# Kernel optimization log

Measured on AMD Instinct MI355X. Metric: run time of the kernel, lower is better.

The kernel has to match this reference:

```python
import jax, jax.numpy as jnp
import numpy as np

S, N, A = 64, 4096, 32
HID, DM, NH, DK = 256, 128, 4, 32
EPS = 1e-5
SCALE = float(np.sqrt(DK))


def setup_inputs() -> dict:
    key = jax.random.key(0)
    ks = jax.random.split(key, 20)
    w = lambda i, sh: jax.random.normal(ks[i], sh, jnp.float32) * 0.02
    z = lambda n: jnp.zeros((n,), jnp.float32)
    return {
        "agent_states": jax.random.normal(ks[0], (N, S), jnp.float32),
        "sw1": w(1, (N * S, HID)), "sb1": z(HID),
        "sw2": w(2, (HID, HID)), "sb2": z(HID),
        "sow": w(3, (HID, 64)), "sob": z(64),
        "tw": w(4, (S + 64, DM)), "tb": z(DM),
        "wq": w(5, (DM, DM)), "bq": z(DM),
        "wk": w(6, (DM, DM)), "bk": z(DM),
        "wv": w(7, (DM, DM)), "bv": z(DM),
        "wo": w(8, (DM, DM)), "bo": z(DM),
        "ln_g": jnp.ones((DM,), jnp.float32), "ln_b": z(DM),
        "taw1": w(9, (DM, 64)), "tab1": z(64),
        "taw2": w(10, (64, 32)), "tab2": z(32),
        "ow1": w(11, (S + DM + 32, 256)), "ob1": z(256),
        "ow2": w(12, (256, DM)), "ob2": z(DM),
        "aw": w(13, (DM, A)), "ab": z(A),
        "vw": w(14, (DM, 1)), "vb": z(1),
        "cw": w(15, (S, 64)), "cb": z(64),
        "cdw": w(16, (64, 32)), "cdb": z(32),
    }


def reference(agent_states, sw1, sb1, sw2, sb2, sow, sob, tw, tb,
              wq, bq, wk, bk, wv, bv, wo, bo, ln_g, ln_b,
              taw1, tab1, taw2, tab2, ow1, ob1, ow2, ob2,
              aw, ab, vw, vb, cw, cb, cdw, cdb):
    n = agent_states.shape[0]
    # strategic level: flatten all agent states -> global objective [64]
    gs = agent_states.reshape(-1)
    strat = jax.nn.relu(jax.nn.relu(gs @ sw1 + sb1) @ sw2 + sb2)
    gobj = strat @ sow + sob
    # tactical encode (batched over agents instead of Python loop)
    tact_in = jnp.concatenate(
        [agent_states, jnp.broadcast_to(gobj, (n, gobj.shape[0]))], axis=-1)
    tact = jax.nn.relu(tact_in @ tw + tb)[None]  # [1, n, DM]
    # multi-head attention across agents
    q = (tact @ wq + bq).reshape(1, n, NH, DK).transpose(0, 2, 1, 3)
    k = (tact @ wk + bk).reshape(1, n, NH, DK).transpose(0, 2, 1, 3)
    v = (tact @ wv + bv).reshape(1, n, NH, DK).transpose(0, 2, 1, 3)
    scores = jnp.einsum('bhqd,bhkd->bhqk', q, k) / SCALE
    attn = jax.nn.softmax(scores, axis=-1)  # [1, NH, n, n]
    ctx = jnp.einsum('bhqk,bhkd->bhqd', attn, v).transpose(0, 2, 1, 3).reshape(1, n, DM)
    res = ctx @ wo + bo + tact
    mu = res.mean(-1, keepdims=True)
    var = res.var(-1, keepdims=True)  # biased, like torch LayerNorm
    coord = ((res - mu) / jnp.sqrt(var + EPS) * ln_g + ln_b)[0]  # [n, DM]
    # task allocation (softmax over 32 tasks)
    task = jax.nn.softmax(jax.nn.relu(coord @ taw1 + tab1) @ taw2 + tab2, axis=-1)
    # operational level -> actions / values
    op_in = jnp.concatenate([agent_states, coord, task], axis=-1)
    opf = jax.nn.relu(jax.nn.relu(op_in @ ow1 + ob1) @ ow2 + ob2)
    actions = opf @ aw + ab
    values = opf @ vw + vb
    # communication messages (two stacked linears, no activation in source)
    messages = (agent_states @ cw + cb) @ cdw + cdb
    return actions, values, messages, task, attn, gobj
```

## Files before the change

kernel.cpp:

```cpp
#include <hip/hip_runtime.h>

typedef __attribute__((ext_vector_type(8))) short s8v;
typedef __attribute__((ext_vector_type(4))) float f4v;

#define MFMA16(a, b, c) __builtin_amdgcn_mfma_f32_16x16x32_bf16((a), (b), (c), 0, 0, 0)

#define NAG   4096
#define SDIM  64
#define DMOD  128
#define NHD   4
#define DKD   32
#define HIDD  256
static constexpr float INV_SCALE = 0.17677669529663687f;
static constexpr float EPSV = 1e-5f;

#define OFF_ACT   0
#define OFF_VAL   131072
#define OFF_MSG   135168
#define OFF_TASK  266240
#define OFF_ATTN  397312
#define OFF_GOBJ  67506176

static constexpr size_t WS_P1   = 0;
static constexpr size_t WS_P1B  = 524288;
static constexpr size_t WS_P2   = 540672;
static constexpr size_t WS_TACT = 558080;
static constexpr size_t WS_Q    = 2655232;
static constexpr size_t WS_K    = 3703808;
static constexpr size_t WS_VT   = 4752384;
static constexpr size_t WS_CTX  = 5800960;
static constexpr size_t WS_OPIN = 7898112;
static constexpr size_t WS_H    = 9733120;
static constexpr size_t WS_OPF  = 11830272;
static constexpr size_t WS_OW1T = 12878848;
static constexpr size_t WS_OW2T = 12993536;

typedef unsigned short u16;
typedef unsigned int   u32;

static __device__ __forceinline__ u16 f2bf(float f) {
    union { float f; u32 u; } x; x.f = f;
    u32 r = x.u + 0x7FFFu + ((x.u >> 16) & 1u);
    return (u16)(r >> 16);
}
static __device__ __forceinline__ float bf2f(u16 b) {
    union { u32 u; float f; } x; x.u = ((u32)b) << 16;
    return x.f;
}

__global__ void kw_prep(const float* __restrict__ ow1, const float* __restrict__ ow2,
                        u16* __restrict__ w1t, u16* __restrict__ w2t) {
    int tid = threadIdx.x;
    int b = blockIdx.x;
    if (b < 224) {
        w1t[tid * 224 + b] = f2bf(ow1[b * 256 + tid]);
    } else {
        if (tid < 128) {
            int k0 = (b - 224) * 8;
#pragma unroll
            for (int kk = 0; kk < 8; ++kk) {
                int k = k0 + kk;
                w2t[tid * 256 + k] = f2bf(ow2[k * 128 + tid]);
            }
        }
    }
}

__global__ __launch_bounds__(256) void k1_sw1(const float* __restrict__ gs,
                                              const float* __restrict__ sw1,
                                              float* __restrict__ p1) {
    __shared__ float gsl[512];
    __shared__ float red[4][256];
    int tid = threadIdx.x;
    int b = blockIdx.x;
    gsl[tid]       = gs[b * 512 + tid];
    gsl[tid + 256] = gs[b * 512 + 256 + tid];
    __syncthreads();
    int t = tid & 63;
    int rg = tid >> 6;
    const f4v* w4 = (const f4v*)sw1;
    f4v acc = {0.f, 0.f, 0.f, 0.f};
    size_t rb = (size_t)b * 512;
#pragma unroll 4
    for (int r = rg; r < 512; r += 4) {
        float g = gsl[r];
        f4v w = __builtin_nontemporal_load(&w4[(rb + r) * 64 + t]);
        acc[0] += g * w[0]; acc[1] += g * w[1]; acc[2] += g * w[2]; acc[3] += g * w[3];
    }
    red[rg][4 * t + 0] = acc[0]; red[rg][4 * t + 1] = acc[1];
    red[rg][4 * t + 2] = acc[2]; red[rg][4 * t + 3] = acc[3];
    __syncthreads();
    float s = red[0][tid] + red[1][tid] + red[2][tid] + red[3][tid];
    p1[b * 256 + tid] = s;
}

__global__ void k1b_red(const float* __restrict__ p1, float* __restrict__ p1b) {
    int j = threadIdx.x;
    int b0 = blockIdx.x * 32;
    float s = 0.f;
#pragma unroll
    for (int b = 0; b < 32; ++b) s += p1[(b0 + b) * 256 + j];
    p1b[blockIdx.x * 256 + j] = s;
}

__global__ void k2b_strat(const float* __restrict__ p1b, const float* __restrict__ sb1,
                          const float* __restrict__ sw2, float* __restrict__ p2) {
    __shared__ float h1[256];
    int j = threadIdx.x;
    float s = 0.f;
#pragma unroll
    for (int b = 0; b < 16; ++b) s += p1b[b * 256 + j];
    h1[j] = fmaxf(s + sb1[j], 0.f);
    __syncthreads();
    int i0 = blockIdx.x * 16;
    float acc = 0.f;
#pragma unroll
    for (int i = 0; i < 16; ++i) acc += h1[i0 + i] * sw2[(i0 + i) * 256 + j];
    p2[blockIdx.x * 256 + j] = acc;
}

__global__ __launch_bounds__(256) void k3_tact_qkv(
    const float* __restrict__ p2, const float* __restrict__ sb2,
    const float* __restrict__ sow, const float* __restrict__ sob,
    const float* __restrict__ as, const float* __restrict__ tw, const float* __restrict__ tb,
    const float* __restrict__ wq, const float* __restrict__ bq,
    const float* __restrict__ wk, const float* __restrict__ bk,
    const float* __restrict__ wv, const float* __restrict__ bv,
    float* __restrict__ out_gobj, float* __restrict__ tactws,
    u16* __restrict__ qws, u16* __restrict__ kws, u16* __restrict__ vtws) {
    __shared__ float strat[256];
    __shared__ float gobj[64];
    __shared__ float asl[16][64];
    __shared__ float tl[16][128];
    int tid = threadIdx.x;
    int a0 = blockIdx.x * 16;
    {
        float s = 0.f;
#pragma unroll
        for (int b = 0; b < 16; ++b) s += p2[b * 256 + tid];
        strat[tid] = fmaxf(s + sb2[tid], 0.f);
    }
#pragma unroll
    for (int r = 0; r < 4; ++r) {
        int idx = tid + r * 256;
        asl[idx >> 6][idx & 63] = as[a0 * 64 + idx];
    }
    __syncthreads();
    if (tid < 64) {
        float g = sob[tid];
        for (int i = 0; i < 256; ++i) g += strat[i] * sow[i * 64 + tid];
        gobj[tid] = g;
        if (blockIdx.x == 0) out_gobj[tid] = g;
    }
    __syncthreads();
    int ah = tid >> 7, j = tid & 127;
    float gacc = 0.f;
    for (int i = 0; i < 64; ++i) gacc += gobj[i] * tw[(64 + i) * 128 + j];
    float acc[8];
    float base = tb[j] + gacc;
#pragma unroll
    for (int a = 0; a < 8; ++a) acc[a] = base;
    for (int i = 0; i < 64; ++i) {
        float w = tw[i * 128 + j];
#pragma unroll
        for (int a = 0; a < 8; ++a) acc[a] += asl[ah * 8 + a][i] * w;
    }
#pragma unroll
    for (int a = 0; a < 8; ++a) {
        float t = fmaxf(acc[a], 0.f);
        tl[ah * 8 + a][j] = t;
        tactws[(size_t)(a0 + ah * 8 + a) * 128 + j] = t;
    }
    __syncthreads();
    int h = j >> 5, d = j & 31;
#pragma unroll
    for (int a = 0; a < 8; ++a) acc[a] = 0.f;
    for (int i = 0; i < 128; ++i) {
        float w = wq[i * 128 + j];
#pragma unroll
        for (int a = 0; a < 8; ++a) acc[a] += tl[ah * 8 + a][i] * w;
    }
#pragma unroll
    for (int a = 0; a < 8; ++a)
        qws[h * 131072 + (a0 + ah * 8 + a) * 32 + d] = f2bf((acc[a] + bq[j]) * INV_SCALE);
#pragma unroll
    for (int a = 0; a < 8; ++a) acc[a] = 0.f;
    for (int i = 0; i < 128; ++i) {
        float w = wk[i * 128 + j];
#pragma unroll
        for (int a = 0; a < 8; ++a) acc[a] += tl[ah * 8 + a][i] * w;
    }
#pragma unroll
    for (int a = 0; a < 8; ++a)
        kws[h * 131072 + (a0 + ah * 8 + a) * 32 + d] = f2bf(acc[a] + bk[j]);
#pragma unroll
    for (int a = 0; a < 8; ++a) acc[a] = 0.f;
    for (int i = 0; i < 128; ++i) {
        float w = wv[i * 128 + j];
#pragma unroll
        for (int a = 0; a < 8; ++a) acc[a] += tl[ah * 8 + a][i] * w;
    }
    union { u16 u[8]; s8v v; } pk;
#pragma unroll
    for (int a = 0; a < 8; ++a) pk.u[a] = f2bf(acc[a] + bv[j]);
    *(s8v*)(vtws + h * 131072 + d * 4096 + a0 + ah * 8) = pk.v;
}

__global__ __launch_bounds__(256) void k4_attn(
    const u16* __restrict__ qws, const u16* __restrict__ kws, const u16* __restrict__ vtws,
    float* __restrict__ attn, float* __restrict__ ctxws) {
    int tid = threadIdx.x;
    int wid = tid >> 6;
    int l = tid & 63;
    int g = l >> 4;
    int ln = l & 15;
    int h = blockIdx.x >> 8;
    int qt = (blockIdx.x & 255) * 16;
    const u16* qh = qws + h * 131072;
    const u16* kh = kws + h * 131072;
    const u16* vh = vtws + h * 131072;
    int j0 = wid * 1024;

    s8v aq = *(const s8v*)(qh + (qt + ln) * 32 + 8 * g);
    f4v zero = {0.f, 0.f, 0.f, 0.f};

    __shared__ float red[4][16];
    __shared__ __align__(16) u16 ldsPb[4][2][16][40];
    __shared__ float pctx[4][16][32];

    f4v lacc = zero, accA = zero, accB = zero;
    int buf = 0;
    for (int jc = 0; jc < 32; ++jc) {
        int jb = j0 + jc * 32;
        s8v b0 = *(const s8v*)(kh + (jb + ln) * 32 + 8 * g);
        s8v b1 = *(const s8v*)(kh + (jb + 16 + ln) * 32 + 8 * g);
        f4v S0 = MFMA16(aq, b0, zero);
        f4v S1 = MFMA16(aq, b1, zero);
#pragma unroll
        for (int r = 0; r < 4; ++r) {
            float w0 = __expf(S0[r]);
            float w1 = __expf(S1[r]);
            lacc[r] += w0 + w1;
            ldsPb[wid][buf][4 * g + r][ln] = f2bf(w0);
            ldsPb[wid][buf][4 * g + r][16 + ln] = f2bf(w1);
        }
        s8v bp = *(const s8v*)&ldsPb[wid][buf][ln][8 * g];
        s8v va = *(const s8v*)(vh + ln * 4096 + jb + 8 * g);
        s8v vb = *(const s8v*)(vh + (16 + ln) * 4096 + jb + 8 * g);
        accA = MFMA16(va, bp, accA);
        accB = MFMA16(vb, bp, accB);
        buf ^= 1;
    }
#pragma unroll
    for (int m = 1; m <= 8; m <<= 1) {
        lacc[0] += __shfl_xor(lacc[0], m);
        lacc[1] += __shfl_xor(lacc[1], m);
        lacc[2] += __shfl_xor(lacc[2], m);
        lacc[3] += __shfl_xor(lacc[3], m);
    }
    if (ln == 0) {
#pragma unroll
        for (int r = 0; r < 4; ++r) red[wid][4 * g + r] = lacc[r];
    }
    __syncthreads();
    float linvr[4];
#pragma unroll
    for (int r = 0; r < 4; ++r) {
        int q = 4 * g + r;
        linvr[r] = 1.f / (red[0][q] + red[1][q] + red[2][q] + red[3][q]);
    }
    float linvq = 1.f / (red[0][ln] + red[1][ln] + red[2][ln] + red[3][ln]);
#pragma unroll
    for (int r = 0; r < 4; ++r) {
        pctx[wid][ln][4 * g + r] = accA[r] * linvq;
        pctx[wid][ln][16 + 4 * g + r] = accB[r] * linvq;
    }
    __syncthreads();
    {
        int q = tid >> 4;
        int dp = tid & 15;
#pragma unroll
        for (int dd = 0; dd < 2; ++dd) {
            int d = dp * 2 + dd;
            float s = pctx[0][q][d] + pctx[1][q][d] + pctx[2][q][d] + pctx[3][q][d];
            ctxws[(size_t)(qt + q) * 128 + h * 32 + d] = s;
        }
    }

    float* attnh = attn + (size_t)h * 4096 * 4096;
    s8v b0 = *(const s8v*)(kh + (j0 + ln) * 32 + 8 * g);
    s8v b1 = *(const s8v*)(kh + (j0 + 16 + ln) * 32 + 8 * g);
    for (int jc = 0; jc < 32; ++jc) {
        int jb = j0 + jc * 32;
        int jn = j0 + ((jc + 1) & 31) * 32;
        s8v n0 = *(const s8v*)(kh + (jn + ln) * 32 + 8 * g);
        s8v n1 = *(const s8v*)(kh + (jn + 16 + ln) * 32 + 8 * g);
        f4v S0 = MFMA16(aq, b0, zero);
        f4v S1 = MFMA16(aq, b1, zero);
#pragma unroll
        for (int r = 0; r < 4; ++r) {
            float w0 = __expf(S0[r]) * linvr[r];
            float w1 = __expf(S1[r]) * linvr[r];
            size_t rowo = ((size_t)(qt + 4 * g + r)) * 4096 + jb;
            attnh[rowo + ln] = w0;
            attnh[rowo + 16 + ln] = w1;
        }
        b0 = n0; b1 = n1;
    }
}

__global__ __launch_bounds__(512) void k5_post(
    const float* __restrict__ ctxws, const float* __restrict__ tactws,
    const float* __restrict__ wo, const float* __restrict__ bo,
    const float* __restrict__ lng, const float* __restrict__ lnb,
    const float* __restrict__ taw1, const float* __restrict__ tab1,
    const float* __restrict__ taw2, const float* __restrict__ tab2,
    const float* __restrict__ as, float* __restrict__ dout, u16* __restrict__ opin) {
    __shared__ float wos[128 * 128];
    __shared__ float tw1s[128 * 64];
    __shared__ float tw2s[64 * 32];
    __shared__ float cx[8][128];
    __shared__ float coords[8][128];
    __shared__ float t1v[8][64];
    int tid = threadIdx.x;
    for (int i = tid; i < 128 * 128; i += 512) wos[i] = wo[i];
    for (int i = tid; i < 128 * 64; i += 512) tw1s[i] = taw1[i];
    for (int i = tid; i < 64 * 32; i += 512) tw2s[i] = taw2[i];
    __syncthreads();
    int w = tid >> 6, l = tid & 63;
    for (int it = 0; it < 2; ++it) {
        int n = blockIdx.x * 16 + w * 2 + it;
        float c0 = ctxws[(size_t)n * 128 + l], c1 = ctxws[(size_t)n * 128 + 64 + l];
        float t0 = tactws[(size_t)n * 128 + l], t1 = tactws[(size_t)n * 128 + 64 + l];
        float av = as[n * 64 + l];
        cx[w][l] = c0; cx[w][64 + l] = c1;
        __syncthreads();
        float r0 = bo[l] + t0, r1 = bo[64 + l] + t1;
        for (int k = 0; k < 128; ++k) {
            float cv = cx[w][k];
            r0 += cv * wos[k * 128 + l];
            r1 += cv * wos[k * 128 + 64 + l];
        }
        float s = r0 + r1;
#pragma unroll
        for (int m = 1; m <= 32; m <<= 1) s += __shfl_xor(s, m);
        float mu = s * (1.f / 128.f);
        float d0 = r0 - mu, d1 = r1 - mu;
        float vs = d0 * d0 + d1 * d1;
#pragma unroll
        for (int m = 1; m <= 32; m <<= 1) vs += __shfl_xor(vs, m);
        float rstd = 1.f / sqrtf(vs * (1.f / 128.f) + EPSV);
        float co0 = d0 * rstd * lng[l] + lnb[l];
        float co1 = d1 * rstd * lng[64 + l] + lnb[64 + l];
        coords[w][l] = co0; coords[w][64 + l] = co1;
        opin[(size_t)n * 224 + l] = f2bf(av);
        opin[(size_t)n * 224 + 64 + l] = f2bf(co0);
        opin[(size_t)n * 224 + 128 + l] = f2bf(co1);
        __syncthreads();
        float a1 = tab1[l];
        for (int i = 0; i < 128; ++i) a1 += coords[w][i] * tw1s[i * 64 + l];
        t1v[w][l] = fmaxf(a1, 0.f);
        __syncthreads();
        if (l < 32) {
            float a2 = tab2[l];
            for (int i = 0; i < 64; ++i) a2 += t1v[w][i] * tw2s[i * 32 + l];
            float mx = a2;
#pragma unroll
            for (int m = 1; m <= 16; m <<= 1) mx = fmaxf(mx, __shfl_xor(mx, m));
            float e = __expf(a2 - mx);
            float se = e;
#pragma unroll
            for (int m = 1; m <= 16; m <<= 1) se += __shfl_xor(se, m);
            float tk = e / se;
            dout[OFF_TASK + n * 32 + l] = tk;
            opin[(size_t)n * 224 + 192 + l] = f2bf(tk);
        }
        __syncthreads();
    }
}

__global__ __launch_bounds__(256) void k6a(const u16* __restrict__ opin, const u16* __restrict__ w1t,
                                           const float* __restrict__ ob1, u16* __restrict__ Hws) {
    int tid = threadIdx.x;
    int w = tid >> 6, l = tid & 63, g = l >> 4, ln = l & 15;
    int bm = blockIdx.x & 63, bn = blockIdx.x >> 6;
    int m0 = bm * 64 + w * 16, n0 = bn * 64;
    f4v acc[4];
    f4v zero = {0.f, 0.f, 0.f, 0.f};
#pragma unroll
    for (int nt = 0; nt < 4; ++nt) acc[nt] = zero;
    for (int kt = 0; kt < 7; ++kt) {
        s8v A = *(const s8v*)(opin + (size_t)(m0 + ln) * 224 + kt * 32 + 8 * g);
#pragma unroll
        for (int nt = 0; nt < 4; ++nt) {
            s8v B = *(const s8v*)(w1t + (size_t)(n0 + nt * 16 + ln) * 224 + kt * 32 + 8 * g);
            acc[nt] = MFMA16(A, B, acc[nt]);
        }
    }
#pragma unroll
    for (int nt = 0; nt < 4; ++nt) {
        int col = n0 + nt * 16 + ln;
        float bias = ob1[col];
#pragma unroll
        for (int r = 0; r < 4; ++r) {
            int row = m0 + 4 * g + r;
            Hws[(size_t)row * 256 + col] = f2bf(fmaxf(acc[nt][r] + bias, 0.f));
        }
    }
}

__global__ __launch_bounds__(256) void k6b(const u16* __restrict__ Hws, const u16* __restrict__ w2t,
                                           const float* __restrict__ ob2, u16* __restrict__ opfws) {
    int tid = threadIdx.x;
    int w = tid >> 6, l = tid & 63, g = l >> 4, ln = l & 15;
    int bm = blockIdx.x & 63, bn = blockIdx.x >> 6;
    int m0 = bm * 64 + w * 16, n0 = bn * 64;
    f4v acc[4];
    f4v zero = {0.f, 0.f, 0.f, 0.f};
#pragma unroll
    for (int nt = 0; nt < 4; ++nt) acc[nt] = zero;
    for (int kt = 0; kt < 8; ++kt) {
        s8v A = *(const s8v*)(Hws + (size_t)(m0 + ln) * 256 + kt * 32 + 8 * g);
#pragma unroll
        for (int nt = 0; nt < 4; ++nt) {
            s8v B = *(const s8v*)(w2t + (size_t)(n0 + nt * 16 + ln) * 256 + kt * 32 + 8 * g);
            acc[nt] = MFMA16(A, B, acc[nt]);
        }
    }
#pragma unroll
    for (int nt = 0; nt < 4; ++nt) {
        int col = n0 + nt * 16 + ln;
        float bias = ob2[col];
#pragma unroll
        for (int r = 0; r < 4; ++r) {
            int row = m0 + 4 * g + r;
            opfws[(size_t)row * 128 + col] = f2bf(fmaxf(acc[nt][r] + bias, 0.f));
        }
    }
}

__global__ __launch_bounds__(256) void k6c(const u16* __restrict__ opf, const float* __restrict__ as,
                                           const float* __restrict__ aw, const float* __restrict__ ab,
                                           const float* __restrict__ vw, const float* __restrict__ vb,
                                           const float* __restrict__ cw, const float* __restrict__ cb,
                                           const float* __restrict__ cdw, const float* __restrict__ cdb,
                                           float* __restrict__ dout) {
    __shared__ float opfs[4][128];
    __shared__ float asl[4][64];
    __shared__ float m1s[4][64];
    int tid = threadIdx.x;
    int w = tid >> 6, l = tid & 63;
    int n = blockIdx.x * 4 + w;
    {
        u32 u = *(const u32*)(opf + (size_t)n * 128 + 2 * l);
        opfs[w][2 * l] = bf2f((u16)(u & 0xffff));
        opfs[w][2 * l + 1] = bf2f((u16)(u >> 16));
        asl[w][l] = as[n * 64 + l];
    }
    __syncthreads();
    if (l < 32) {
        float a = ab[l];
        for (int k = 0; k < 128; ++k) a += opfs[w][k] * aw[k * 32 + l];
        dout[OFF_ACT + n * 32 + l] = a;
    }
    {
        float p = opfs[w][l] * vw[l] + opfs[w][64 + l] * vw[64 + l];
#pragma unroll
        for (int m = 1; m <= 32; m <<= 1) p += __shfl_xor(p, m);
        if (l == 0) dout[OFF_VAL + n] = p + vb[0];
    }
    {
        float a = cb[l];
        for (int k = 0; k < 64; ++k) a += asl[w][k] * cw[k * 64 + l];
        m1s[w][l] = a;
    }
    __syncthreads();
    if (l < 32) {
        float a = cdb[l];
        for (int k = 0; k < 64; ++k) a += m1s[w][k] * cdw[k * 32 + l];
        dout[OFF_MSG + n * 32 + l] = a;
    }
}

extern "C" void kernel_launch(void* const* d_in, const int* in_sizes, int n_in,
                              void* d_out, int out_size, void* d_ws, size_t ws_size,
                              hipStream_t stream) {
    const float* as  = (const float*)d_in[0];
    const float* sw1 = (const float*)d_in[1];
    const float* sb1 = (const float*)d_in[2];
    const float* sw2 = (const float*)d_in[3];
    const float* sb2 = (const float*)d_in[4];
    const float* sow = (const float*)d_in[5];
    const float* sob = (const float*)d_in[6];
    const float* tw  = (const float*)d_in[7];
    const float* tb  = (const float*)d_in[8];
    const float* wq  = (const float*)d_in[9];
    const float* bq  = (const float*)d_in[10];
    const float* wk  = (const float*)d_in[11];
    const float* bk  = (const float*)d_in[12];
    const float* wv  = (const float*)d_in[13];
    const float* bv  = (const float*)d_in[14];
    const float* wo  = (const float*)d_in[15];
    const float* bo  = (const float*)d_in[16];
    const float* lng = (const float*)d_in[17];
    const float* lnb = (const float*)d_in[18];
    const float* taw1 = (const float*)d_in[19];
    const float* tab1 = (const float*)d_in[20];
    const float* taw2 = (const float*)d_in[21];
    const float* tab2 = (const float*)d_in[22];
    const float* ow1 = (const float*)d_in[23];
    const float* ob1 = (const float*)d_in[24];
    const float* ow2 = (const float*)d_in[25];
    const float* ob2 = (const float*)d_in[26];
    const float* aw  = (const float*)d_in[27];
    const float* ab  = (const float*)d_in[28];
    const float* vw  = (const float*)d_in[29];
    const float* vb  = (const float*)d_in[30];
    const float* cw  = (const float*)d_in[31];
    const float* cb  = (const float*)d_in[32];
    const float* cdw = (const float*)d_in[33];
    const float* cdb = (const float*)d_in[34];

    float* dout = (float*)d_out;
    char* ws = (char*)d_ws;
    float* p1    = (float*)(ws + WS_P1);
    float* p1b   = (float*)(ws + WS_P1B);
    float* p2    = (float*)(ws + WS_P2);
    float* tactw = (float*)(ws + WS_TACT);
    u16*   qws   = (u16*)(ws + WS_Q);
    u16*   kws   = (u16*)(ws + WS_K);
    u16*   vtws  = (u16*)(ws + WS_VT);
    float* ctxws = (float*)(ws + WS_CTX);
    u16*   opin  = (u16*)(ws + WS_OPIN);
    u16*   Hws   = (u16*)(ws + WS_H);
    u16*   opfws = (u16*)(ws + WS_OPF);
    u16*   w1t   = (u16*)(ws + WS_OW1T);
    u16*   w2t   = (u16*)(ws + WS_OW2T);

    hipLaunchKernelGGL(kw_prep, dim3(256), dim3(256), 0, stream, ow1, ow2, w1t, w2t);
    hipLaunchKernelGGL(k1_sw1, dim3(512), dim3(256), 0, stream, as, sw1, p1);
    hipLaunchKernelGGL(k1b_red, dim3(16), dim3(256), 0, stream, p1, p1b);
    hipLaunchKernelGGL(k2b_strat, dim3(16), dim3(256), 0, stream, p1b, sb1, sw2, p2);
    hipLaunchKernelGGL(k3_tact_qkv, dim3(256), dim3(256), 0, stream,
                       p2, sb2, sow, sob, as, tw, tb, wq, bq, wk, bk, wv, bv,
                       dout + OFF_GOBJ, tactw, qws, kws, vtws);
    hipLaunchKernelGGL(k4_attn, dim3(1024), dim3(256), 0, stream,
                       qws, kws, vtws, dout + OFF_ATTN, ctxws);
    hipLaunchKernelGGL(k5_post, dim3(256), dim3(512), 0, stream,
                       ctxws, tactw, wo, bo, lng, lnb, taw1, tab1, taw2, tab2, as, dout, opin);
    hipLaunchKernelGGL(k6a, dim3(256), dim3(256), 0, stream, opin, w1t, ob1, Hws);
    hipLaunchKernelGGL(k6b, dim3(128), dim3(256), 0, stream, Hws, w2t, ob2, opfws);
    hipLaunchKernelGGL(k6c, dim3(1024), dim3(256), 0, stream,
                       opfws, as, aw, ab, vw, vb, cw, cb, cdw, cdb, dout);
}
```

Measured before the change: 214.8 us.

## Fuse weight prep into sw1 kernel, drop reduce kernel, vectorize attn stores

Folds the ow1/ow2 bf16 transpose prep into extra blocks of the sw1 GEMV kernel. It removes the intermediate partial-sum reduction kernel, so k2b_strat now sums all 512 partials directly. In the attention-probability write loop, the MFMA operand order is swapped so each lane holds four consecutive key columns of one query row, which allows 16-byte vector stores instead of scattered scalar stores. This cuts two launches and should improve store coalescing on the large attn output. The cost is that each of the 16 k2b blocks redundantly reads 512x256 partials.

```diff
diff --git a/kernel.cpp b/kernel.cpp
--- a/kernel.cpp
+++ b/kernel.cpp
@@ -48,31 +48,31 @@
     return x.f;
 }
 
-__global__ void kw_prep(const float* __restrict__ ow1, const float* __restrict__ ow2,
-                        u16* __restrict__ w1t, u16* __restrict__ w2t) {
+__global__ __launch_bounds__(256) void k1_sw1(const float* __restrict__ gs,
+                                              const float* __restrict__ sw1,
+                                              float* __restrict__ p1,
+                                              const float* __restrict__ ow1,
+                                              const float* __restrict__ ow2,
+                                              u16* __restrict__ w1t,
+                                              u16* __restrict__ w2t) {
     int tid = threadIdx.x;
     int b = blockIdx.x;
-    if (b < 224) {
-        w1t[tid * 224 + b] = f2bf(ow1[b * 256 + tid]);
-    } else {
-        if (tid < 128) {
-            int k0 = (b - 224) * 8;
+    if (b >= 512) {
+        int bb = b - 512;
+        if (bb < 224) {
+            w1t[tid * 224 + bb] = f2bf(ow1[bb * 256 + tid]);
+        } else if (tid < 128) {
+            int k0 = (bb - 224) * 8;
 #pragma unroll
             for (int kk = 0; kk < 8; ++kk) {
                 int k = k0 + kk;
                 w2t[tid * 256 + k] = f2bf(ow2[k * 128 + tid]);
             }
         }
-    }
-}
-
-__global__ __launch_bounds__(256) void k1_sw1(const float* __restrict__ gs,
-                                              const float* __restrict__ sw1,
-                                              float* __restrict__ p1) {
+        return;
+    }
     __shared__ float gsl[512];
     __shared__ float red[4][256];
-    int tid = threadIdx.x;
-    int b = blockIdx.x;
     gsl[tid]       = gs[b * 512 + tid];
     gsl[tid + 256] = gs[b * 512 + 256 + tid];
     __syncthreads();
@@ -94,22 +94,13 @@
     p1[b * 256 + tid] = s;
 }
 
-__global__ void k1b_red(const float* __restrict__ p1, float* __restrict__ p1b) {
-    int j = threadIdx.x;
-    int b0 = blockIdx.x * 32;
-    float s = 0.f;
-#pragma unroll
-    for (int b = 0; b < 32; ++b) s += p1[(b0 + b) * 256 + j];
-    p1b[blockIdx.x * 256 + j] = s;
-}
-
-__global__ void k2b_strat(const float* __restrict__ p1b, const float* __restrict__ sb1,
+__global__ void k2b_strat(const float* __restrict__ p1, const float* __restrict__ sb1,
                           const float* __restrict__ sw2, float* __restrict__ p2) {
     __shared__ float h1[256];
     int j = threadIdx.x;
     float s = 0.f;
-#pragma unroll
-    for (int b = 0; b < 16; ++b) s += p1b[b * 256 + j];
+#pragma unroll 8
+    for (int b = 0; b < 512; ++b) s += p1[b * 256 + j];
     h1[j] = fmaxf(s + sb1[j], 0.f);
     __syncthreads();
     int i0 = blockIdx.x * 16;
@@ -263,12 +254,6 @@
         for (int r = 0; r < 4; ++r) red[wid][4 * g + r] = lacc[r];
     }
     __syncthreads();
-    float linvr[4];
-#pragma unroll
-    for (int r = 0; r < 4; ++r) {
-        int q = 4 * g + r;
-        linvr[r] = 1.f / (red[0][q] + red[1][q] + red[2][q] + red[3][q]);
-    }
     float linvq = 1.f / (red[0][ln] + red[1][ln] + red[2][ln] + red[3][ln]);
 #pragma unroll
     for (int r = 0; r < 4; ++r) {
@@ -287,7 +272,7 @@
         }
     }
 
-    float* attnh = attn + (size_t)h * 4096 * 4096;
+    float* rowp = attn + (size_t)h * 4096 * 4096 + (size_t)(qt + ln) * 4096;
     s8v b0 = *(const s8v*)(kh + (j0 + ln) * 32 + 8 * g);
     s8v b1 = *(const s8v*)(kh + (j0 + 16 + ln) * 32 + 8 * g);
     for (int jc = 0; jc < 32; ++jc) {
@@ -295,16 +280,16 @@
         int jn = j0 + ((jc + 1) & 31) * 32;
         s8v n0 = *(const s8v*)(kh + (jn + ln) * 32 + 8 * g);
         s8v n1 = *(const s8v*)(kh + (jn + 16 + ln) * 32 + 8 * g);
-        f4v S0 = MFMA16(aq, b0, zero);
-        f4v S1 = MFMA16(aq, b1, zero);
+        f4v S0 = MFMA16(b0, aq, zero);
+        f4v S1 = MFMA16(b1, aq, zero);
+        f4v o0, o1;
 #pragma unroll
         for (int r = 0; r < 4; ++r) {
-            float w0 = __expf(S0[r]) * linvr[r];
-            float w1 = __expf(S1[r]) * linvr[r];
-            size_t rowo = ((size_t)(qt + 4 * g + r)) * 4096 + jb;
-            attnh[rowo + ln] = w0;
-            attnh[rowo + 16 + ln] = w1;
-        }
+            o0[r] = __expf(S0[r]) * linvq;
+            o1[r] = __expf(S1[r]) * linvq;
+        }
+        *(f4v*)(rowp + jb + 4 * g) = o0;
+        *(f4v*)(rowp + jb + 16 + 4 * g) = o1;
         b0 = n0; b1 = n1;
     }
 }
@@ -524,7 +509,6 @@
     float* dout = (float*)d_out;
     char* ws = (char*)d_ws;
     float* p1    = (float*)(ws + WS_P1);
-    float* p1b   = (float*)(ws + WS_P1B);
     float* p2    = (float*)(ws + WS_P2);
     float* tactw = (float*)(ws + WS_TACT);
     u16*   qws   = (u16*)(ws + WS_Q);
@@ -537,10 +521,8 @@
     u16*   w1t   = (u16*)(ws + WS_OW1T);
     u16*   w2t   = (u16*)(ws + WS_OW2T);
 
-    hipLaunchKernelGGL(kw_prep, dim3(256), dim3(256), 0, stream, ow1, ow2, w1t, w2t);
-    hipLaunchKernelGGL(k1_sw1, dim3(512), dim3(256), 0, stream, as, sw1, p1);
-    hipLaunchKernelGGL(k1b_red, dim3(16), dim3(256), 0, stream, p1, p1b);
-    hipLaunchKernelGGL(k2b_strat, dim3(16), dim3(256), 0, stream, p1b, sb1, sw2, p2);
+    hipLaunchKernelGGL(k1_sw1, dim3(768), dim3(256), 0, stream, as, sw1, p1, ow1, ow2, w1t, w2t);
+    hipLaunchKernelGGL(k2b_strat, dim3(16), dim3(256), 0, stream, p1, sb1, sw2, p2);
     hipLaunchKernelGGL(k3_tact_qkv, dim3(256), dim3(256), 0, stream,
                        p2, sb2, sow, sob, as, tw, tb, wq, bq, wk, bk, wv, bv,
                        dout + OFF_GOBJ, tactw, qws, kws, vtws);
```

Measured after the change: 238.3 us. 11.0% more time.
